# Optimization experiments

Measured on AMD Instinct MI355X. Metric: run time of the kernel, lower is better.

The kernel has to match this reference:

```python
import jax, jax.numpy as jnp
import numpy as np

C = 256
R = 8
CR = C // R  # 32


def setup_inputs() -> dict:
    key = jax.random.key(0)
    kx, kq, kk, kv = jax.random.split(key, 4)
    x = jax.random.normal(kx, (4, C, 64, 64), dtype=jnp.float32)
    # 1x1 conv weights, no bias: [out_ch, in_ch]
    Wq = jax.random.normal(kq, (CR, C), dtype=jnp.float32) * (1.0 / np.sqrt(C))
    Wk = jax.random.normal(kk, (CR, C), dtype=jnp.float32) * (1.0 / np.sqrt(C))
    Wv = jax.random.normal(kv, (C, C), dtype=jnp.float32) * (1.0 / np.sqrt(C))
    return {"x": x, "Wq": Wq, "Wk": Wk, "Wv": Wv}


def reference(x, Wq, Wk, Wv):
    B, Cc, H, W = x.shape
    N = H * W
    xf = x.reshape(B, Cc, N)                      # [B, C, N]
    q = jnp.einsum('oc,bcn->bno', Wq, xf)         # [B, N, Cr]
    k = jnp.einsum('oc,bcn->bon', Wk, xf)         # [B, Cr, N]
    v = jnp.einsum('oc,bcn->bon', Wv, xf)         # [B, C, N]
    energy = jnp.einsum('bno,bom->bnm', q, k)     # [B, N, N]
    attn = jax.nn.softmax(energy, axis=-1)
    out = jnp.einsum('bcm,bnm->bcn', v, attn)     # [B, C, N]
    return out.reshape(B, Cc, H, W) + x
```

## Files before the change

kernel.cpp:

```cpp
#include <hip/hip_runtime.h>
#include <stdint.h>
#include <stddef.h>

#define Bn 4
#define Cn 256
#define CRn 32
#define Nn 4096

typedef __attribute__((ext_vector_type(8))) short short8v;
typedef __attribute__((ext_vector_type(4))) float f32x4;

__device__ __forceinline__ unsigned short f2bf(float f) {
  unsigned int u = __float_as_uint(f);
  u += 0x7FFFu + ((u >> 16) & 1u);
  return (unsigned short)(u >> 16);
}

__global__ void __launch_bounds__(256) k_wcast(const float* __restrict__ Wq,
                                               const float* __restrict__ Wk,
                                               const float* __restrict__ Wv,
                                               unsigned short* __restrict__ Wb) {
  int idx = (blockIdx.x * 256 + threadIdx.x) * 4;
  int row = idx >> 8, cc = idx & 255;
  const float* src = (row < 32) ? &Wq[row * 256 + cc]
                   : (row < 64) ? &Wk[(row - 32) * 256 + cc]
                                : &Wv[(row - 64) * 256 + cc];
  float4 f = *reinterpret_cast<const float4*>(src);
  ushort4 o;
  o.x = f2bf(f.x); o.y = f2bf(f.y); o.z = f2bf(f.z); o.w = f2bf(f.w);
  *reinterpret_cast<ushort4*>(&Wb[idx]) = o;
}

__global__ void __launch_bounds__(512) k_proj(const unsigned short* __restrict__ Wb,
                                              const float* __restrict__ x,
                                              unsigned short* __restrict__ Qt,
                                              unsigned short* __restrict__ Kt,
                                              unsigned short* __restrict__ V) {
  __shared__ __align__(16) unsigned char smem[50432];
  unsigned short* xs = (unsigned short*)smem;
  float* xf = (float*)(smem + 33792);
  unsigned short* vb = (unsigned short*)smem;
  const int t  = threadIdx.x;
  const int nt = blockIdx.x, b = blockIdx.y;
  const int li = t & 15, cr = t >> 4;

  for (int ct = 0; ct < 4; ++ct) {
    if (ct) __syncthreads();
#pragma unroll
    for (int p = 0; p < 2; ++p) {
      int c = cr + (p << 5);
      float4 f = *reinterpret_cast<const float4*>(
          &x[(((size_t)((b << 8) + (ct << 6) + c)) << 12) + (nt << 6) + (li << 2)]);
      xf[c * 65 + (li << 2) + 0] = f.x;
      xf[c * 65 + (li << 2) + 1] = f.y;
      xf[c * 65 + (li << 2) + 2] = f.z;
      xf[c * 65 + (li << 2) + 3] = f.w;
    }
    __syncthreads();
#pragma unroll
    for (int p = 0; p < 2; ++p) {
      int nl = cr + (p << 5);
      int cq = li << 2;
      ushort4 o;
      o.x = f2bf(xf[(cq + 0) * 65 + nl]);
      o.y = f2bf(xf[(cq + 1) * 65 + nl]);
      o.z = f2bf(xf[(cq + 2) * 65 + nl]);
      o.w = f2bf(xf[(cq + 3) * 65 + nl]);
      *reinterpret_cast<ushort4*>(&xs[nl * 264 + (ct << 6) + cq]) = o;
    }
  }
  __syncthreads();

  const int lane = t & 63, w = t >> 6, col = lane & 15, hi = lane >> 4;
  const int nw = w & 3, rh = w >> 2;
  f32x4 zero4 = {0.f, 0.f, 0.f, 0.f};
  f32x4 acc[10];
#pragma unroll
  for (int rc = 0; rc < 10; ++rc) acc[rc] = zero4;

#pragma unroll
  for (int ks = 0; ks < 8; ++ks) {
    short8v af = *reinterpret_cast<const short8v*>(
        &xs[((nw << 4) + col) * 264 + (ks << 5) + (hi << 3)]);
#pragma unroll
    for (int rc = 0; rc < 10; ++rc) {
      short8v bf = *reinterpret_cast<const short8v*>(
          Wb + (((size_t)(rh * 160 + (rc << 4) + col)) << 8) + (ks << 5) + (hi << 3));
      acc[rc] = __builtin_amdgcn_mfma_f32_16x16x32_bf16(af, bf, acc[rc], 0, 0, 0);
    }
  }

  if (rh == 0) {
#pragma unroll
    for (int rc = 0; rc < 2; ++rc)
#pragma unroll
      for (int r = 0; r < 4; ++r) {
        int n = (nt << 6) + (nw << 4) + (hi << 2) + r;
        Qt[(((size_t)((b << 12) + n)) << 5) + (rc << 4) + col] = f2bf(acc[rc][r]);
      }
#pragma unroll
    for (int rc = 2; rc < 4; ++rc)
#pragma unroll
      for (int r = 0; r < 4; ++r) {
        int n = (nt << 6) + (nw << 4) + (hi << 2) + r;
        Kt[(((size_t)((b << 12) + n)) << 5) + ((rc - 2) << 4) + col] = f2bf(acc[rc][r]);
      }
  }
  __syncthreads();

  {
    const int rcStart = (rh == 0) ? 4 : 0;
    const int nb = (nw << 4) + (hi << 2);
#pragma unroll
    for (int rc = 0; rc < 10; ++rc) {
      if (rc < rcStart) continue;
      int c = rh * 160 + (rc << 4) + col - 64;
#pragma unroll
      for (int r = 0; r < 4; ++r)
        vb[c * 72 + nb + r] = f2bf(acc[rc][r]);
    }
  }
  __syncthreads();

#pragma unroll
  for (int p = 0; p < 4; ++p) {
    int idx = (p << 9) + t;
    int c = idx >> 3, off = idx & 7;
    int offp = off ^ (c & 7);
    int4 dv = *reinterpret_cast<const int4*>(&vb[c * 72 + (offp << 3)]);
    *reinterpret_cast<int4*>(
        &V[(((size_t)((b << 8) + c)) << 12) + (nt << 6) + (offp << 3)]) = dv;
  }
}

__global__ void __launch_bounds__(512, 4) k_attn(const unsigned short* __restrict__ Qt,
                                                 const unsigned short* __restrict__ Kt,
                                                 const unsigned short* __restrict__ Vv,
                                                 const float* __restrict__ x,
                                                 float* __restrict__ out) {
  __shared__ unsigned short Qs[64][40];
  __shared__ __align__(16) unsigned short Pt[2][2][64 * 64];
  __shared__ float Sc[2][2][64];
  __shared__ float Mm[2][64], Ll[2][64];
  __shared__ float Ob[4][16][64];

  const int t = threadIdx.x, bx = blockIdx.x;
  const int xcd = bx & 7;
  const int b = xcd >> 1, ch = xcd & 1;
  const int qt = bx >> 3;
  const int lane = t & 63, w = t >> 6, col = lane & 15, hi = lane >> 4;
  const int g = w >> 2, wg = w & 3;
  const int cBase = (ch << 7) + (wg << 5);

  if (t < 256) {
    const int mr = t >> 2, u = t & 3;
    int4 d = *reinterpret_cast<const int4*>(
        Qt + (((size_t)((b << 12) + (qt << 6) + mr)) << 5) + (u << 3));
    *reinterpret_cast<int4*>(&Qs[mr][u << 3]) = d;
  }

  const unsigned short* KtB = Kt + (((size_t)(b << 12)) << 5);
  const unsigned short* VvB = Vv + (((size_t)((b << 8) + cBase)) << 12);

  const int kt0 = g << 5;
  int m0 = kt0 << 6;
  short8v kf[4], vf[4];
#pragma unroll
  for (int mb = 0; mb < 4; ++mb)
    kf[mb] = *reinterpret_cast<const short8v*>(
        KtB + (((size_t)(m0 + (mb << 4) + col)) << 5) + (hi << 3));
#pragma unroll
  for (int ks = 0; ks < 2; ++ks)
#pragma unroll
    for (int cb = 0; cb < 2; ++cb)
      vf[(ks << 1) + cb] = *reinterpret_cast<const short8v*>(
          VvB + (((size_t)((cb << 4) + col)) << 12) + m0 + (ks << 5) + (hi << 3));
  __syncthreads();
  const short8v qf = *reinterpret_cast<const short8v*>(&Qs[(wg << 4) + col][hi << 3]);

  f32x4 zero4 = {0.f, 0.f, 0.f, 0.f};
  f32x4 o_acc[2][4];
#pragma unroll
  for (int cb = 0; cb < 2; ++cb)
#pragma unroll
    for (int nc = 0; nc < 4; ++nc) o_acc[cb][nc] = zero4;
  float m_run = -3e38f, l_run = 0.f;

#pragma unroll 1
  for (int i = 0; i < 32; ++i) {
    const int p = i & 1;
    const int iNext = (i < 31) ? (i + 1) : 31;
    const int mN = (kt0 + iNext) << 6;

    f32x4 s_acc[4];
#pragma unroll
    for (int mb = 0; mb < 4; ++mb)
      s_acc[mb] = __builtin_amdgcn_mfma_f32_16x16x32_bf16(kf[mb], qf, zero4, 0, 0, 0);
#pragma unroll
    for (int mb = 0; mb < 4; ++mb)
      kf[mb] = *reinterpret_cast<const short8v*>(
          KtB + (((size_t)(mN + (mb << 4) + col)) << 5) + (hi << 3));

    float tm = -3e38f;
#pragma unroll
    for (int mb = 0; mb < 4; ++mb)
#pragma unroll
      for (int r = 0; r < 4; ++r) tm = fmaxf(tm, s_acc[mb][r]);
    tm = fmaxf(tm, __shfl_xor(tm, 16));
    tm = fmaxf(tm, __shfl_xor(tm, 32));
    float mn = fmaxf(m_run, tm);
    float sc = __expf(m_run - mn);
    m_run = mn;
    float ps = 0.f;
#pragma unroll
    for (int mb = 0; mb < 4; ++mb)
#pragma unroll
      for (int r = 0; r < 4; ++r) {
        float pv = __expf(s_acc[mb][r] - mn);
        s_acc[mb][r] = pv;
        ps += pv;
      }
    ps += __shfl_xor(ps, 16);
    ps += __shfl_xor(ps, 32);
    l_run = l_run * sc + ps;
    if (hi == 0) Sc[g][p][(wg << 4) + col] = sc;
#pragma unroll
    for (int mb = 0; mb < 4; ++mb) {
      uint2 pk2;
      pk2.x = (unsigned)f2bf(s_acc[mb][0]) | ((unsigned)f2bf(s_acc[mb][1]) << 16);
      pk2.y = (unsigned)f2bf(s_acc[mb][2]) | ((unsigned)f2bf(s_acc[mb][3]) << 16);
      int uu = (mb << 1) + (hi >> 1);
      int up = uu ^ (col & 7);
      *reinterpret_cast<uint2*>(
          &Pt[g][p][(((wg << 4) + col) << 6) + (up << 3) + ((hi & 1) << 2)]) = pk2;
    }

    asm volatile("s_waitcnt lgkmcnt(0)" ::: "memory");
    __builtin_amdgcn_s_barrier();

    float scl[4];
#pragma unroll
    for (int nc = 0; nc < 4; ++nc) scl[nc] = Sc[g][p][(nc << 4) + col];
#pragma unroll
    for (int cb = 0; cb < 2; ++cb)
#pragma unroll
      for (int nc = 0; nc < 4; ++nc) o_acc[cb][nc] *= scl[nc];
#pragma unroll
    for (int ks = 0; ks < 2; ++ks) {
      short8v pb[4];
      int up2 = ((ks << 2) + hi) ^ (col & 7);
#pragma unroll
      for (int nc = 0; nc < 4; ++nc)
        pb[nc] = *reinterpret_cast<const short8v*>(
            &Pt[g][p][(((nc << 4) + col) << 6) + (up2 << 3)]);
#pragma unroll
      for (int cb = 0; cb < 2; ++cb)
#pragma unroll
        for (int nc = 0; nc < 4; ++nc)
          o_acc[cb][nc] = __builtin_amdgcn_mfma_f32_16x16x32_bf16(
              vf[(ks << 1) + cb], pb[nc], o_acc[cb][nc], 0, 0, 0);
    }
#pragma unroll
    for (int ks = 0; ks < 2; ++ks)
#pragma unroll
      for (int cb = 0; cb < 2; ++cb)
        vf[(ks << 1) + cb] = *reinterpret_cast<const short8v*>(
            VvB + (((size_t)((cb << 4) + col)) << 12) + mN + (ks << 5) + (hi << 3));
  }

  if (hi == 0) { Mm[g][(wg << 4) + col] = m_run; Ll[g][(wg << 4) + col] = l_run; }
  __syncthreads();
  float fa[4], fb[4], linv[4];
#pragma unroll
  for (int nc = 0; nc < 4; ++nc) {
    float ma = Mm[0][(nc << 4) + col], mb2 = Mm[1][(nc << 4) + col];
    float mm = fmaxf(ma, mb2);
    float ea = __expf(ma - mm), eb = __expf(mb2 - mm);
    linv[nc] = 1.f / (Ll[0][(nc << 4) + col] * ea + Ll[1][(nc << 4) + col] * eb);
    fa[nc] = ea; fb[nc] = eb;
  }
#pragma unroll
  for (int cb = 0; cb < 2; ++cb) {
    if (g == 1) {
#pragma unroll
      for (int nc = 0; nc < 4; ++nc)
#pragma unroll
        for (int r = 0; r < 4; ++r)
          Ob[wg][(nc << 2) + r][lane] = o_acc[cb][nc][r];
    }
    __syncthreads();
    if (g == 0) {
#pragma unroll
      for (int nc = 0; nc < 4; ++nc)
#pragma unroll
        for (int r = 0; r < 4; ++r) {
          float o = o_acc[cb][nc][r] * fa[nc] + Ob[wg][(nc << 2) + r][lane] * fb[nc];
          int cg = cBase + (cb << 4) + (hi << 2) + r;
          int ng = (qt << 6) + (nc << 4) + col;
          size_t off = (((size_t)((b << 8) + cg)) << 12) + ng;
          out[off] = o * linv[nc] + x[off];
        }
    }
    __syncthreads();
  }
}

extern "C" void kernel_launch(void* const* d_in, const int* in_sizes, int n_in,
                              void* d_out, int out_size, void* d_ws, size_t ws_size,
                              hipStream_t stream) {
  (void)in_sizes; (void)n_in; (void)out_size; (void)ws_size;
  const float* x  = (const float*)d_in[0];
  const float* Wq = (const float*)d_in[1];
  const float* Wk = (const float*)d_in[2];
  const float* Wv = (const float*)d_in[3];
  float* out = (float*)d_out;

  unsigned short* Qt = (unsigned short*)d_ws;
  unsigned short* Kt = Qt + (size_t)Bn * Nn * CRn;
  unsigned short* Vv = Kt + (size_t)Bn * Nn * CRn;
  unsigned short* Wb = Vv + (size_t)Bn * Cn * Nn;

  hipLaunchKernelGGL(k_wcast, dim3(80),        dim3(256), 0, stream, Wq, Wk, Wv, Wb);
  hipLaunchKernelGGL(k_proj,  dim3(64, 4),     dim3(512), 0, stream, Wb, x, Qt, Kt, Vv);
  hipLaunchKernelGGL(k_attn,  dim3(512),       dim3(512), 0, stream, Qt, Kt, Vv, x, out);
}
```

Before: 190.2 us.

## Split projection rows across blocks and stage weights in LDS with double-buffering

The projection kernel now splits the 320 output rows (Q, K, V) across two blocks per spatial tile, so the grid doubles and each wave keeps 5 accumulators instead of 10. Each k-step's weight slice is async-copied into a swizzled, double-buffered LDS buffer with global_load_lds, replacing per-wave direct global reads of the weights. The attention kernel's launch bounds change from 4 to 2 blocks per CU, which loosens register limits. In exchange, the x tile is loaded and converted twice (once per row block), and each k-step now ends with a block barrier.

```diff
diff --git a/kernel.cpp b/kernel.cpp
--- a/kernel.cpp
+++ b/kernel.cpp
@@ -36,12 +36,15 @@
                                               unsigned short* __restrict__ Qt,
                                               unsigned short* __restrict__ Kt,
                                               unsigned short* __restrict__ V) {
-  __shared__ __align__(16) unsigned char smem[50432];
-  unsigned short* xs = (unsigned short*)smem;
-  float* xf = (float*)(smem + 33792);
-  unsigned short* vb = (unsigned short*)smem;
+  __shared__ __align__(16) unsigned char smem[54272];
+  unsigned short* xs   = (unsigned short*)smem;
+  unsigned short* wbuf = (unsigned short*)(smem + 33792);
+  float*          xf   = (float*)(smem + 33792);
+  unsigned short* vb   = (unsigned short*)smem;
+
   const int t  = threadIdx.x;
-  const int nt = blockIdx.x, b = blockIdx.y;
+  const int nt = blockIdx.x, rt = blockIdx.y, b = blockIdx.z;
+  const int rbase = rt * 160;
   const int li = t & 15, cr = t >> 4;
 
   for (int ct = 0; ct < 4; ++ct) {
@@ -71,26 +74,50 @@
   }
   __syncthreads();
 
+  auto STAGEWB = [&](int ks, int buf) {
+#pragma unroll
+    for (int r = 0; r < 2; ++r) {
+      int idx = (r << 9) + t;
+      if (idx < 640) {
+        int row = idx >> 2, seg = idx & 3;
+        int sseg = seg ^ ((row ^ (row >> 2)) & 3);
+        const unsigned short* g =
+            Wb + (((size_t)(rbase + row)) << 8) + (ks << 5) + (sseg << 3);
+        __builtin_amdgcn_global_load_lds(
+            (const __attribute__((address_space(1))) void*)g,
+            (__attribute__((address_space(3))) void*)(wbuf + buf * 5120 + idx * 8),
+            16, 0, 0);
+      }
+    }
+  };
+
+  STAGEWB(0, 0);
+  __syncthreads();
+
   const int lane = t & 63, w = t >> 6, col = lane & 15, hi = lane >> 4;
-  const int nw = w & 3, rh = w >> 2;
+  const int nw = w & 3, rh2 = w >> 2;
   f32x4 zero4 = {0.f, 0.f, 0.f, 0.f};
-  f32x4 acc[10];
-#pragma unroll
-  for (int rc = 0; rc < 10; ++rc) acc[rc] = zero4;
-
-#pragma unroll
+  f32x4 acc[5];
+#pragma unroll
+  for (int rc = 0; rc < 5; ++rc) acc[rc] = zero4;
+
+#pragma unroll 1
   for (int ks = 0; ks < 8; ++ks) {
+    const unsigned short* wB = wbuf + (ks & 1) * 5120;
+    if (ks < 7) STAGEWB(ks + 1, (ks & 1) ^ 1);
     short8v af = *reinterpret_cast<const short8v*>(
         &xs[((nw << 4) + col) * 264 + (ks << 5) + (hi << 3)]);
 #pragma unroll
-    for (int rc = 0; rc < 10; ++rc) {
-      short8v bf = *reinterpret_cast<const short8v*>(
-          Wb + (((size_t)(rh * 160 + (rc << 4) + col)) << 8) + (ks << 5) + (hi << 3));
+    for (int rc = 0; rc < 5; ++rc) {
+      int row = rh2 * 80 + (rc << 4) + col;
+      int sw = hi ^ ((row ^ (row >> 2)) & 3);
+      short8v bf = *reinterpret_cast<const short8v*>(wB + row * 32 + (sw << 3));
       acc[rc] = __builtin_amdgcn_mfma_f32_16x16x32_bf16(af, bf, acc[rc], 0, 0, 0);
     }
-  }
-
-  if (rh == 0) {
+    __syncthreads();
+  }
+
+  if (rt == 0 && rh2 == 0) {
 #pragma unroll
     for (int rc = 0; rc < 2; ++rc)
 #pragma unroll
@@ -106,34 +133,39 @@
         Kt[(((size_t)((b << 12) + n)) << 5) + ((rc - 2) << 4) + col] = f2bf(acc[rc][r]);
       }
   }
-  __syncthreads();
-
+
+  const int nch = rt ? 160 : 96;
   {
-    const int rcStart = (rh == 0) ? 4 : 0;
     const int nb = (nw << 4) + (hi << 2);
-#pragma unroll
-    for (int rc = 0; rc < 10; ++rc) {
-      if (rc < rcStart) continue;
-      int c = rh * 160 + (rc << 4) + col - 64;
-#pragma unroll
-      for (int r = 0; r < 4; ++r)
-        vb[c * 72 + nb + r] = f2bf(acc[rc][r]);
-    }
-  }
-  __syncthreads();
-
-#pragma unroll
-  for (int p = 0; p < 4; ++p) {
+    const int sub = (rt == 0) ? 64 : 0;
+#pragma unroll
+    for (int rc = 0; rc < 5; ++rc) {
+      int grow_l = rh2 * 80 + (rc << 4) + col;
+      int ch_l = grow_l - sub;
+      if (ch_l >= 0) {
+#pragma unroll
+        for (int r = 0; r < 4; ++r)
+          vb[ch_l * 72 + nb + r] = f2bf(acc[rc][r]);
+      }
+    }
+  }
+  __syncthreads();
+
+  const int cgBase = rt ? 96 : 0;
+#pragma unroll
+  for (int p = 0; p < 3; ++p) {
     int idx = (p << 9) + t;
-    int c = idx >> 3, off = idx & 7;
-    int offp = off ^ (c & 7);
-    int4 dv = *reinterpret_cast<const int4*>(&vb[c * 72 + (offp << 3)]);
-    *reinterpret_cast<int4*>(
-        &V[(((size_t)((b << 8) + c)) << 12) + (nt << 6) + (offp << 3)]) = dv;
-  }
-}
-
-__global__ void __launch_bounds__(512, 4) k_attn(const unsigned short* __restrict__ Qt,
+    if (idx < nch * 8) {
+      int c = idx >> 3, off = idx & 7;
+      int offp = off ^ (c & 7);
+      int4 dv = *reinterpret_cast<const int4*>(&vb[c * 72 + (offp << 3)]);
+      *reinterpret_cast<int4*>(
+          &V[(((size_t)((b << 8) + cgBase + c)) << 12) + (nt << 6) + (offp << 3)]) = dv;
+    }
+  }
+}
+
+__global__ void __launch_bounds__(512, 2) k_attn(const unsigned short* __restrict__ Qt,
                                                  const unsigned short* __restrict__ Kt,
                                                  const unsigned short* __restrict__ Vv,
                                                  const float* __restrict__ x,
@@ -321,6 +353,6 @@
   unsigned short* Wb = Vv + (size_t)Bn * Cn * Nn;
 
   hipLaunchKernelGGL(k_wcast, dim3(80),        dim3(256), 0, stream, Wq, Wk, Wv, Wb);
-  hipLaunchKernelGGL(k_proj,  dim3(64, 4),     dim3(512), 0, stream, Wb, x, Qt, Kt, Vv);
+  hipLaunchKernelGGL(k_proj,  dim3(64, 2, 4),  dim3(512), 0, stream, Wb, x, Qt, Kt, Vv);
   hipLaunchKernelGGL(k_attn,  dim3(512),       dim3(512), 0, stream, Qt, Kt, Vv, x, out);
 }
```

Result: faster. 175.2 us (-7.8%).
